# Optimization experiments

Hardware: AMD Instinct MI355X
Metric: run time of the kernel (lower is better)

The kernel has to match this reference:

```python
import jax, jax.numpy as jnp
import numpy as np

EPS = 0.01                      # cfg.eps
INV_4PI = 1.0 / (4.0 * np.pi)   # 3D free-space Green's constant


def setup_inputs() -> dict:
    key = jax.random.key(0)
    k1, k2, k3 = jax.random.split(key, 3)
    B, M, d = 32768, 2048, 3
    return {
        "x_query": jax.random.normal(k1, (B, d), dtype=jnp.float32),
        "x_land": jax.random.normal(k2, (M, d), dtype=jnp.float32),
        "g_land": jax.random.normal(k3, (M,), dtype=jnp.float32),
    }


def reference(x_query, x_land, g_land):
    # Regularized 3D Poisson Green's function:
    #   G(x,y)      =  1/(4*pi) * (||x-y||^2 + eps^2)^(-1/2)
    #   grad_x G    = -1/(4*pi) * (x-y) * (||x-y||^2 + eps^2)^(-3/2)
    M = x_land.shape[0]
    r2 = (jnp.sum(x_query * x_query, axis=1)[:, None]
          - 2.0 * (x_query @ x_land.T)
          + jnp.sum(x_land * x_land, axis=1)[None, :])
    t = jnp.maximum(r2, 0.0) + EPS * EPS          # (B, M), regularized
    G = INV_4PI * jax.lax.rsqrt(t)                # (B, M)
    v_hat = (G * g_land[None, :]).sum(axis=1) / M # (B,)
    # fused gradient reduction: avoid materializing (B, M, d) dG.
    # sum_m g_m * dG = -1/(4pi) * [ x_q * sum_m c_m  -  c @ x_land ],
    # where c_m = g_m * t^(-3/2)
    c = g_land[None, :] * t ** (-1.5)             # (B, M)
    gradv_hat = -INV_4PI * (x_query * c.sum(axis=1, keepdims=True) - c @ x_land) / M
    return v_hat, gradv_hat
```

## Files before the change

### kernel.cpp

```cpp
#include <hip/hip_runtime.h>
#include <math.h>


#define EPS2    1e-4f
#define INV_4PI 0.07957747154594767f

constexpr int M_LAND = 2048;
constexpr int NW     = 16;
constexpr int SLICE  = M_LAND / NW;
constexpr int QPB    = 128;

typedef float f32x2 __attribute__((ext_vector_type(2)));

__global__ __launch_bounds__(1024, 4)
void poisson_pk_kernel(const float* __restrict__ xq,
                       const float* __restrict__ xl,
                       const float* __restrict__ gl,
                       float* __restrict__ out, int B)
{
    __shared__ float4 pack[M_LAND];
    __shared__ float4 gpack[M_LAND];
    __shared__ float  part[NW][QPB][5];

    const int tid = threadIdx.x;

    for (int j = tid; j < M_LAND; j += 1024) {
        float l0 = xl[3*j], l1 = xl[3*j+1], l2 = xl[3*j+2], g = gl[j];
        float n2 = l0*l0 + l1*l1 + l2*l2 + EPS2;
        pack[j]  = make_float4(-2.0f*l0, -2.0f*l1, -2.0f*l2, n2);
        gpack[j] = make_float4(-2.0f*g*l0, -2.0f*g*l1, -2.0f*g*l2, g);
    }

    const int lane  = tid & 63;
    const int w     = tid >> 6;
    const int qbase = blockIdx.x * QPB;
    const int qa    = qbase + lane;
    const int qb    = qbase + 64 + lane;

    const float a0 = xq[3*qa], a1 = xq[3*qa+1], a2 = xq[3*qa+2];
    const float b0 = xq[3*qb], b1 = xq[3*qb+1], b2 = xq[3*qb+2];

    f32x2 Q0 = {a0, b0}, Q1 = {a1, b1}, Q2 = {a2, b2};
    f32x2 QE = {a0*a0 + a1*a1 + a2*a2, b0*b0 + b1*b1 + b2*b2};
    f32x2 AV = {0.f,0.f}, AC = {0.f,0.f}, AX = {0.f,0.f}, AY = {0.f,0.f}, AZ = {0.f,0.f};

    __syncthreads();

    const int base = w * SLICE;
#pragma unroll 8
    for (int i = 0; i < SLICE; ++i) {
        const float4 p  = pack[base + i];
        const float4 gp = gpack[base + i];
        f32x2 P01 = {p.x,  p.y};
        f32x2 P2W = {p.z,  p.w};
        f32x2 G01 = {gp.x, gp.y};
        f32x2 G2G = {gp.z, gp.w};

        f32x2 T;
        asm("v_pk_add_f32 %0, %1, %2 op_sel:[0,1] op_sel_hi:[1,1]\n\t"
            "v_pk_fma_f32 %0, %2, %3, %0 op_sel:[0,0,0] op_sel_hi:[0,1,1]\n\t"
            "v_pk_fma_f32 %0, %4, %5, %0 op_sel:[1,0,0] op_sel_hi:[1,1,1]\n\t"
            "v_pk_fma_f32 %0, %4, %6, %0 op_sel:[0,0,0] op_sel_hi:[0,1,1]"
            : "=&v"(T)
            : "v"(QE), "v"(P2W), "v"(Q2), "v"(P01), "v"(Q1), "v"(Q0));

        float ta = fmaxf(T.x, EPS2);
        float tb = fmaxf(T.y, EPS2);
        f32x2 S = { __builtin_amdgcn_rsqf(ta), __builtin_amdgcn_rsqf(tb) };

        f32x2 S2, S3;
        asm("v_pk_mul_f32 %0, %7, %7 op_sel:[0,0] op_sel_hi:[1,1]\n\t"
            "v_pk_mul_f32 %1, %0, %7 op_sel:[0,0] op_sel_hi:[1,1]\n\t"
            "v_pk_fma_f32 %2, %8, %7, %2 op_sel:[1,0,0] op_sel_hi:[1,1,1]\n\t"
            "v_pk_fma_f32 %3, %8, %1, %3 op_sel:[1,0,0] op_sel_hi:[1,1,1]\n\t"
            "v_pk_fma_f32 %4, %1, %9, %4 op_sel:[0,0,0] op_sel_hi:[1,0,1]\n\t"
            "v_pk_fma_f32 %5, %1, %9, %5 op_sel:[0,1,0] op_sel_hi:[1,1,1]\n\t"
            "v_pk_fma_f32 %6, %1, %8, %6 op_sel:[0,0,0] op_sel_hi:[1,0,1]"
            : "=&v"(S2), "=&v"(S3),
              "+v"(AV), "+v"(AC), "+v"(AX), "+v"(AY), "+v"(AZ)
            : "v"(S), "v"(G2G), "v"(G01));
    }

    part[w][lane][0] = AV.x;  part[w][lane][1] = AC.x;
    part[w][lane][2] = AX.x;  part[w][lane][3] = AY.x;  part[w][lane][4] = AZ.x;
    part[w][lane+64][0] = AV.y;  part[w][lane+64][1] = AC.y;
    part[w][lane+64][2] = AX.y;  part[w][lane+64][3] = AY.y;  part[w][lane+64][4] = AZ.y;

    __syncthreads();

    if (tid < 512) {
        const int q   = tid >> 2;
        const int cmp = tid & 3;
        const int qg  = qbase + q;
        if (cmp == 0) {
            float s = 0.f;
            #pragma unroll
            for (int ww = 0; ww < NW; ++ww) s += part[ww][q][0];
            out[qg] = s * (INV_4PI / (float)M_LAND);
        } else {
            float sc = 0.f, sy = 0.f;
            #pragma unroll
            for (int ww = 0; ww < NW; ++ww) {
                sc += part[ww][q][1];
                sy += part[ww][q][1 + cmp];
            }
            const float qc = xq[3*qg + (cmp-1)];
            out[B + 3*qg + (cmp-1)] =
                (-INV_4PI / (float)M_LAND) * fmaf(qc, sc, 0.5f * sy);
        }
    }
}

extern "C" void kernel_launch(void* const* d_in, const int* in_sizes, int n_in,
                              void* d_out, int out_size, void* d_ws, size_t ws_size,
                              hipStream_t stream)
{
    const float* xq = (const float*)d_in[0];
    const float* xl = (const float*)d_in[1];
    const float* gl = (const float*)d_in[2];
    float* out = (float*)d_out;

    const int B    = in_sizes[0] / 3;
    const int grid = B / QPB;

    poisson_pk_kernel<<<grid, 1024, 0, stream>>>(xq, xl, gl, out, B);
}
```

Baseline: 26.91 us.

## Store raw landmarks in one shared array and recompute norms per iteration

Drops the second shared-memory array of pre-scaled g*l values and the precomputed landmark norm. The -2 factor moves onto the query side, and each landmark's squared norm is recomputed inside the inner loop. Accumulation switches from inline-asm packed FMA to scalar code. This halves LDS reads and LDS footprint per iteration but adds about three FMAs per landmark plus extra scalar multiplies, and it gives up the explicit packed-math instructions.

```diff
diff --git a/kernel.cpp b/kernel.cpp
--- a/kernel.cpp
+++ b/kernel.cpp
@@ -13,23 +13,17 @@
 typedef float f32x2 __attribute__((ext_vector_type(2)));
 
 __global__ __launch_bounds__(1024, 4)
-void poisson_pk_kernel(const float* __restrict__ xq,
+void poisson_r7_kernel(const float* __restrict__ xq,
                        const float* __restrict__ xl,
                        const float* __restrict__ gl,
                        float* __restrict__ out, int B)
 {
     __shared__ float4 pack[M_LAND];
-    __shared__ float4 gpack[M_LAND];
     __shared__ float  part[NW][QPB][5];
 
     const int tid = threadIdx.x;
-
-    for (int j = tid; j < M_LAND; j += 1024) {
-        float l0 = xl[3*j], l1 = xl[3*j+1], l2 = xl[3*j+2], g = gl[j];
-        float n2 = l0*l0 + l1*l1 + l2*l2 + EPS2;
-        pack[j]  = make_float4(-2.0f*l0, -2.0f*l1, -2.0f*l2, n2);
-        gpack[j] = make_float4(-2.0f*g*l0, -2.0f*g*l1, -2.0f*g*l2, g);
-    }
+    for (int j = tid; j < M_LAND; j += 1024)
+        pack[j] = make_float4(xl[3*j], xl[3*j+1], xl[3*j+2], gl[j]);
 
     const int lane  = tid & 63;
     const int w     = tid >> 6;
@@ -40,51 +34,53 @@
     const float a0 = xq[3*qa], a1 = xq[3*qa+1], a2 = xq[3*qa+2];
     const float b0 = xq[3*qb], b1 = xq[3*qb+1], b2 = xq[3*qb+2];
 
-    f32x2 Q0 = {a0, b0}, Q1 = {a1, b1}, Q2 = {a2, b2};
-    f32x2 QE = {a0*a0 + a1*a1 + a2*a2, b0*b0 + b1*b1 + b2*b2};
-    f32x2 AV = {0.f,0.f}, AC = {0.f,0.f}, AX = {0.f,0.f}, AY = {0.f,0.f}, AZ = {0.f,0.f};
+    f32x2 Qn0 = {-2.0f*a0, -2.0f*b0};
+    f32x2 Qn1 = {-2.0f*a1, -2.0f*b1};
+    f32x2 Qn2 = {-2.0f*a2, -2.0f*b2};
+    f32x2 QE  = {a0*a0 + a1*a1 + a2*a2, b0*b0 + b1*b1 + b2*b2};
+
+    float av_a=0.f, ac_a=0.f, ax_a=0.f, ay_a=0.f, az_a=0.f;
+    float av_b=0.f, ac_b=0.f, ax_b=0.f, ay_b=0.f, az_b=0.f;
 
     __syncthreads();
 
     const int base = w * SLICE;
 #pragma unroll 8
     for (int i = 0; i < SLICE; ++i) {
-        const float4 p  = pack[base + i];
-        const float4 gp = gpack[base + i];
-        f32x2 P01 = {p.x,  p.y};
-        f32x2 P2W = {p.z,  p.w};
-        f32x2 G01 = {gp.x, gp.y};
-        f32x2 G2G = {gp.z, gp.w};
+        const float4 p = pack[base + i];
+        f32x2 P01 = {p.x, p.y};
+        f32x2 P2G = {p.z, p.w};
+
+        float n2 = fmaf(p.x, p.x, fmaf(p.y, p.y, fmaf(p.z, p.z, EPS2)));
 
         f32x2 T;
-        asm("v_pk_add_f32 %0, %1, %2 op_sel:[0,1] op_sel_hi:[1,1]\n\t"
-            "v_pk_fma_f32 %0, %2, %3, %0 op_sel:[0,0,0] op_sel_hi:[0,1,1]\n\t"
+        asm("v_pk_fma_f32 %0, %1, %2, %3 op_sel:[0,0,0] op_sel_hi:[0,1,1]\n\t"
             "v_pk_fma_f32 %0, %4, %5, %0 op_sel:[1,0,0] op_sel_hi:[1,1,1]\n\t"
             "v_pk_fma_f32 %0, %4, %6, %0 op_sel:[0,0,0] op_sel_hi:[0,1,1]"
             : "=&v"(T)
-            : "v"(QE), "v"(P2W), "v"(Q2), "v"(P01), "v"(Q1), "v"(Q0));
+            : "v"(P2G), "v"(Qn2), "v"(QE), "v"(P01), "v"(Qn1), "v"(Qn0));
 
-        float ta = fmaxf(T.x, EPS2);
-        float tb = fmaxf(T.y, EPS2);
-        f32x2 S = { __builtin_amdgcn_rsqf(ta), __builtin_amdgcn_rsqf(tb) };
+        float ta = fmaxf(T.x + n2, EPS2);
+        float tb = fmaxf(T.y + n2, EPS2);
+        float sa = __builtin_amdgcn_rsqf(ta);
+        float sb = __builtin_amdgcn_rsqf(tb);
 
-        f32x2 S2, S3;
-        asm("v_pk_mul_f32 %0, %7, %7 op_sel:[0,0] op_sel_hi:[1,1]\n\t"
-            "v_pk_mul_f32 %1, %0, %7 op_sel:[0,0] op_sel_hi:[1,1]\n\t"
-            "v_pk_fma_f32 %2, %8, %7, %2 op_sel:[1,0,0] op_sel_hi:[1,1,1]\n\t"
-            "v_pk_fma_f32 %3, %8, %1, %3 op_sel:[1,0,0] op_sel_hi:[1,1,1]\n\t"
-            "v_pk_fma_f32 %4, %1, %9, %4 op_sel:[0,0,0] op_sel_hi:[1,0,1]\n\t"
-            "v_pk_fma_f32 %5, %1, %9, %5 op_sel:[0,1,0] op_sel_hi:[1,1,1]\n\t"
-            "v_pk_fma_f32 %6, %1, %8, %6 op_sel:[0,0,0] op_sel_hi:[1,0,1]"
-            : "=&v"(S2), "=&v"(S3),
-              "+v"(AV), "+v"(AC), "+v"(AX), "+v"(AY), "+v"(AZ)
-            : "v"(S), "v"(G2G), "v"(G01));
+        float s3a = sa * sa * sa;
+        float s3b = sb * sb * sb;
+        float ca  = p.w * s3a;
+        float cb  = p.w * s3b;
+
+        av_a = fmaf(p.w, sa, av_a);   av_b = fmaf(p.w, sb, av_b);
+        ac_a += ca;                   ac_b += cb;
+        ax_a = fmaf(ca, p.x, ax_a);   ax_b = fmaf(cb, p.x, ax_b);
+        ay_a = fmaf(ca, p.y, ay_a);   ay_b = fmaf(cb, p.y, ay_b);
+        az_a = fmaf(ca, p.z, az_a);   az_b = fmaf(cb, p.z, az_b);
     }
 
-    part[w][lane][0] = AV.x;  part[w][lane][1] = AC.x;
-    part[w][lane][2] = AX.x;  part[w][lane][3] = AY.x;  part[w][lane][4] = AZ.x;
-    part[w][lane+64][0] = AV.y;  part[w][lane+64][1] = AC.y;
-    part[w][lane+64][2] = AX.y;  part[w][lane+64][3] = AY.y;  part[w][lane+64][4] = AZ.y;
+    part[w][lane][0] = av_a;  part[w][lane][1] = ac_a;
+    part[w][lane][2] = ax_a;  part[w][lane][3] = ay_a;  part[w][lane][4] = az_a;
+    part[w][lane+64][0] = av_b;  part[w][lane+64][1] = ac_b;
+    part[w][lane+64][2] = ax_b;  part[w][lane+64][3] = ay_b;  part[w][lane+64][4] = az_b;
 
     __syncthreads();
 
@@ -106,7 +102,7 @@
             }
             const float qc = xq[3*qg + (cmp-1)];
             out[B + 3*qg + (cmp-1)] =
-                (-INV_4PI / (float)M_LAND) * fmaf(qc, sc, 0.5f * sy);
+                (-INV_4PI / (float)M_LAND) * fmaf(qc, sc, -sy);
         }
     }
 }
@@ -123,5 +119,5 @@
     const int B    = in_sizes[0] / 3;
     const int grid = B / QPB;
 
-    poisson_pk_kernel<<<grid, 1024, 0, stream>>>(xq, xl, gl, out, B);
+    poisson_r7_kernel<<<grid, 1024, 0, stream>>>(xq, xl, gl, out, B);
 }
```

After: 31.22 us. 16.0% more time.

## Split landmark dimension across blocks with workspace partials and a combine kernel

Applied to the files above, without the earlier changes.

The work is now split into two kernels. The first gives each block 256 queries and one quarter of the landmarks, with every thread handling four queries, and writes reduced partial sums to the workspace. A second small kernel adds the four landmark-slice partials and forms the value and gradient outputs. The aim is to raise per-thread ILP, shrink the per-block shared-memory staging, and fill the GPU with 512 smaller blocks. The cost is an extra launch and a global-memory round trip, and the new path only runs when B equals 32768 and the workspace is large enough; otherwise the original kernel is used.

```diff
diff --git a/kernel.cpp b/kernel.cpp
--- a/kernel.cpp
+++ b/kernel.cpp
@@ -6,101 +6,199 @@
 #define INV_4PI 0.07957747154594767f
 
 constexpr int M_LAND = 2048;
-constexpr int NW     = 16;
-constexpr int SLICE  = M_LAND / NW;
-constexpr int QPB    = 128;
 
 typedef float f32x2 __attribute__((ext_vector_type(2)));
 
-__global__ __launch_bounds__(1024, 4)
-void poisson_pk_kernel(const float* __restrict__ xq,
-                       const float* __restrict__ xl,
-                       const float* __restrict__ gl,
-                       float* __restrict__ out, int B)
-{
-    __shared__ float4 pack[M_LAND];
-    __shared__ float4 gpack[M_LAND];
-    __shared__ float  part[NW][QPB][5];
-
-    const int tid = threadIdx.x;
-
-    for (int j = tid; j < M_LAND; j += 1024) {
-        float l0 = xl[3*j], l1 = xl[3*j+1], l2 = xl[3*j+2], g = gl[j];
+#define PAIR_COMPUTE(Q0_, Q1_, Q2_, QE_, AV_, AC_, AX_, AY_, AZ_) do { \
+    f32x2 T; \
+    asm("v_pk_add_f32 %0, %1, %2 op_sel:[0,1] op_sel_hi:[1,1]\n\t" \
+        "v_pk_fma_f32 %0, %2, %3, %0 op_sel:[0,0,0] op_sel_hi:[0,1,1]\n\t" \
+        "v_pk_fma_f32 %0, %4, %5, %0 op_sel:[1,0,0] op_sel_hi:[1,1,1]\n\t" \
+        "v_pk_fma_f32 %0, %4, %6, %0 op_sel:[0,0,0] op_sel_hi:[0,1,1]" \
+        : "=&v"(T) \
+        : "v"(QE_), "v"(P2W), "v"(Q2_), "v"(P01), "v"(Q1_), "v"(Q0_)); \
+    float ta = fmaxf(T.x, EPS2); \
+    float tb = fmaxf(T.y, EPS2); \
+    f32x2 S = { __builtin_amdgcn_rsqf(ta), __builtin_amdgcn_rsqf(tb) }; \
+    f32x2 S2, S3; \
+    asm("v_pk_mul_f32 %0, %7, %7 op_sel:[0,0] op_sel_hi:[1,1]\n\t" \
+        "v_pk_mul_f32 %1, %0, %7 op_sel:[0,0] op_sel_hi:[1,1]\n\t" \
+        "v_pk_fma_f32 %2, %8, %7, %2 op_sel:[1,0,0] op_sel_hi:[1,1,1]\n\t" \
+        "v_pk_fma_f32 %3, %8, %1, %3 op_sel:[1,0,0] op_sel_hi:[1,1,1]\n\t" \
+        "v_pk_fma_f32 %4, %1, %9, %4 op_sel:[0,0,0] op_sel_hi:[1,0,1]\n\t" \
+        "v_pk_fma_f32 %5, %1, %9, %5 op_sel:[0,1,0] op_sel_hi:[1,1,1]\n\t" \
+        "v_pk_fma_f32 %6, %1, %8, %6 op_sel:[0,0,0] op_sel_hi:[1,0,1]" \
+        : "=&v"(S2), "=&v"(S3), \
+          "+v"(AV_), "+v"(AC_), "+v"(AX_), "+v"(AY_), "+v"(AZ_) \
+        : "v"(S), "v"(G2G), "v"(G01)); \
+} while (0)
+
+__global__ __launch_bounds__(512, 4)
+void poisson_part_kernel(const float* __restrict__ xq,
+                         const float* __restrict__ xl,
+                         const float* __restrict__ gl,
+                         float* __restrict__ ws)
+{
+    __shared__ float4 pack[512];
+    __shared__ float4 gpack[512];
+    __shared__ float  part[8][256][5];
+
+    const int tid  = threadIdx.x;
+    const int qblk = blockIdx.x >> 2;
+    const int ms   = blockIdx.x & 3;
+
+    {
+        int jg = ms * 512 + tid;
+        float l0 = xl[3*jg], l1 = xl[3*jg+1], l2 = xl[3*jg+2], g = gl[jg];
         float n2 = l0*l0 + l1*l1 + l2*l2 + EPS2;
-        pack[j]  = make_float4(-2.0f*l0, -2.0f*l1, -2.0f*l2, n2);
-        gpack[j] = make_float4(-2.0f*g*l0, -2.0f*g*l1, -2.0f*g*l2, g);
+        pack[tid]  = make_float4(-2.0f*l0, -2.0f*l1, -2.0f*l2, n2);
+        gpack[tid] = make_float4(-2.0f*g*l0, -2.0f*g*l1, -2.0f*g*l2, g);
     }
 
     const int lane  = tid & 63;
     const int w     = tid >> 6;
-    const int qbase = blockIdx.x * QPB;
-    const int qa    = qbase + lane;
-    const int qb    = qbase + 64 + lane;
+    const int qbase = qblk * 256;
+
+    const int qa = qbase + lane,       qbq = qbase + 64  + lane;
+    const int qc = qbase + 128 + lane, qd  = qbase + 192 + lane;
 
     const float a0 = xq[3*qa], a1 = xq[3*qa+1], a2 = xq[3*qa+2];
-    const float b0 = xq[3*qb], b1 = xq[3*qb+1], b2 = xq[3*qb+2];
-
-    f32x2 Q0 = {a0, b0}, Q1 = {a1, b1}, Q2 = {a2, b2};
-    f32x2 QE = {a0*a0 + a1*a1 + a2*a2, b0*b0 + b1*b1 + b2*b2};
-    f32x2 AV = {0.f,0.f}, AC = {0.f,0.f}, AX = {0.f,0.f}, AY = {0.f,0.f}, AZ = {0.f,0.f};
-
-    __syncthreads();
-
-    const int base = w * SLICE;
-#pragma unroll 8
-    for (int i = 0; i < SLICE; ++i) {
+    const float b0 = xq[3*qbq], b1 = xq[3*qbq+1], b2 = xq[3*qbq+2];
+    const float c0 = xq[3*qc], c1 = xq[3*qc+1], c2 = xq[3*qc+2];
+    const float d0 = xq[3*qd], d1 = xq[3*qd+1], d2 = xq[3*qd+2];
+
+    f32x2 Q0a = {a0, b0}, Q1a = {a1, b1}, Q2a = {a2, b2};
+    f32x2 QEa = {a0*a0 + a1*a1 + a2*a2, b0*b0 + b1*b1 + b2*b2};
+    f32x2 Q0b = {c0, d0}, Q1b = {c1, d1}, Q2b = {c2, d2};
+    f32x2 QEb = {c0*c0 + c1*c1 + c2*c2, d0*d0 + d1*d1 + d2*d2};
+
+    f32x2 AVa = {0,0}, ACa = {0,0}, AXa = {0,0}, AYa = {0,0}, AZa = {0,0};
+    f32x2 AVb = {0,0}, ACb = {0,0}, AXb = {0,0}, AYb = {0,0}, AZb = {0,0};
+
+    __syncthreads();
+
+    const int base = w * 64;
+#pragma unroll 4
+    for (int i = 0; i < 64; ++i) {
         const float4 p  = pack[base + i];
         const float4 gp = gpack[base + i];
         f32x2 P01 = {p.x,  p.y};
         f32x2 P2W = {p.z,  p.w};
         f32x2 G01 = {gp.x, gp.y};
         f32x2 G2G = {gp.z, gp.w};
-
-        f32x2 T;
-        asm("v_pk_add_f32 %0, %1, %2 op_sel:[0,1] op_sel_hi:[1,1]\n\t"
-            "v_pk_fma_f32 %0, %2, %3, %0 op_sel:[0,0,0] op_sel_hi:[0,1,1]\n\t"
-            "v_pk_fma_f32 %0, %4, %5, %0 op_sel:[1,0,0] op_sel_hi:[1,1,1]\n\t"
-            "v_pk_fma_f32 %0, %4, %6, %0 op_sel:[0,0,0] op_sel_hi:[0,1,1]"
-            : "=&v"(T)
-            : "v"(QE), "v"(P2W), "v"(Q2), "v"(P01), "v"(Q1), "v"(Q0));
-
-        float ta = fmaxf(T.x, EPS2);
-        float tb = fmaxf(T.y, EPS2);
-        f32x2 S = { __builtin_amdgcn_rsqf(ta), __builtin_amdgcn_rsqf(tb) };
-
-        f32x2 S2, S3;
-        asm("v_pk_mul_f32 %0, %7, %7 op_sel:[0,0] op_sel_hi:[1,1]\n\t"
-            "v_pk_mul_f32 %1, %0, %7 op_sel:[0,0] op_sel_hi:[1,1]\n\t"
-            "v_pk_fma_f32 %2, %8, %7, %2 op_sel:[1,0,0] op_sel_hi:[1,1,1]\n\t"
-            "v_pk_fma_f32 %3, %8, %1, %3 op_sel:[1,0,0] op_sel_hi:[1,1,1]\n\t"
-            "v_pk_fma_f32 %4, %1, %9, %4 op_sel:[0,0,0] op_sel_hi:[1,0,1]\n\t"
-            "v_pk_fma_f32 %5, %1, %9, %5 op_sel:[0,1,0] op_sel_hi:[1,1,1]\n\t"
-            "v_pk_fma_f32 %6, %1, %8, %6 op_sel:[0,0,0] op_sel_hi:[1,0,1]"
-            : "=&v"(S2), "=&v"(S3),
-              "+v"(AV), "+v"(AC), "+v"(AX), "+v"(AY), "+v"(AZ)
-            : "v"(S), "v"(G2G), "v"(G01));
-    }
-
+        PAIR_COMPUTE(Q0a, Q1a, Q2a, QEa, AVa, ACa, AXa, AYa, AZa);
+        PAIR_COMPUTE(Q0b, Q1b, Q2b, QEb, AVb, ACb, AXb, AYb, AZb);
+    }
+
+    part[w][lane][0] = AVa.x;  part[w][lane][1] = ACa.x;
+    part[w][lane][2] = AXa.x;  part[w][lane][3] = AYa.x;  part[w][lane][4] = AZa.x;
+    part[w][lane+64][0] = AVa.y;  part[w][lane+64][1] = ACa.y;
+    part[w][lane+64][2] = AXa.y;  part[w][lane+64][3] = AYa.y;  part[w][lane+64][4] = AZa.y;
+    part[w][lane+128][0] = AVb.x;  part[w][lane+128][1] = ACb.x;
+    part[w][lane+128][2] = AXb.x;  part[w][lane+128][3] = AYb.x;  part[w][lane+128][4] = AZb.x;
+    part[w][lane+192][0] = AVb.y;  part[w][lane+192][1] = ACb.y;
+    part[w][lane+192][2] = AXb.y;  part[w][lane+192][3] = AYb.y;  part[w][lane+192][4] = AZb.y;
+
+    __syncthreads();
+
+    for (int s = tid; s < 1280; s += 512) {
+        const int comp = s >> 8;
+        const int qloc = s & 255;
+        float acc = 0.f;
+        #pragma unroll
+        for (int ww = 0; ww < 8; ++ww) acc += part[ww][qloc][comp];
+        ws[(size_t)blockIdx.x * 1280 + s] = acc;
+    }
+}
+
+__global__ __launch_bounds__(512)
+void poisson_combine_kernel(const float* __restrict__ ws,
+                            const float* __restrict__ xq,
+                            float* __restrict__ out, int B)
+{
+    const int gid  = blockIdx.x * 512 + threadIdx.x;
+    const int q    = gid >> 2;
+    const int cmp  = gid & 3;
+    const int qblk = q >> 8;
+    const int qloc = q & 255;
+    const float* wbase = ws + (size_t)qblk * 4 * 1280;
+
+    if (cmp == 0) {
+        float s = 0.f;
+        #pragma unroll
+        for (int m = 0; m < 4; ++m) s += wbase[m*1280 + qloc];
+        out[q] = s * (INV_4PI / (float)M_LAND);
+    } else {
+        float sc = 0.f, sy = 0.f;
+        #pragma unroll
+        for (int m = 0; m < 4; ++m) {
+            sc += wbase[m*1280 + 256 + qloc];
+            sy += wbase[m*1280 + (1+cmp)*256 + qloc];
+        }
+        const float qc = xq[3*q + (cmp-1)];
+        out[B + 3*q + (cmp-1)] =
+            (-INV_4PI / (float)M_LAND) * fmaf(qc, sc, 0.5f * sy);
+    }
+}
+
+constexpr int NW_F  = 16;
+constexpr int SL_F  = M_LAND / NW_F;
+constexpr int QPB_F = 128;
+
+__global__ __launch_bounds__(1024, 4)
+void poisson_pk_kernel(const float* __restrict__ xq,
+                       const float* __restrict__ xl,
+                       const float* __restrict__ gl,
+                       float* __restrict__ out, int B)
+{
+    __shared__ float4 pack[M_LAND];
+    __shared__ float4 gpack[M_LAND];
+    __shared__ float  part[NW_F][QPB_F][5];
+
+    const int tid = threadIdx.x;
+    for (int j = tid; j < M_LAND; j += 1024) {
+        float l0 = xl[3*j], l1 = xl[3*j+1], l2 = xl[3*j+2], g = gl[j];
+        float n2 = l0*l0 + l1*l1 + l2*l2 + EPS2;
+        pack[j]  = make_float4(-2.0f*l0, -2.0f*l1, -2.0f*l2, n2);
+        gpack[j] = make_float4(-2.0f*g*l0, -2.0f*g*l1, -2.0f*g*l2, g);
+    }
+    const int lane = tid & 63, w = tid >> 6;
+    const int qbase = blockIdx.x * QPB_F;
+    const int qa = qbase + lane, qb = qbase + 64 + lane;
+    const float a0 = xq[3*qa], a1 = xq[3*qa+1], a2 = xq[3*qa+2];
+    const float b0 = xq[3*qb], b1 = xq[3*qb+1], b2 = xq[3*qb+2];
+    f32x2 Q0 = {a0, b0}, Q1 = {a1, b1}, Q2 = {a2, b2};
+    f32x2 QE = {a0*a0 + a1*a1 + a2*a2, b0*b0 + b1*b1 + b2*b2};
+    f32x2 AV = {0,0}, AC = {0,0}, AX = {0,0}, AY = {0,0}, AZ = {0,0};
+    __syncthreads();
+
+    const int base = w * SL_F;
+#pragma unroll 8
+    for (int i = 0; i < SL_F; ++i) {
+        const float4 p  = pack[base + i];
+        const float4 gp = gpack[base + i];
+        f32x2 P01 = {p.x,  p.y};
+        f32x2 P2W = {p.z,  p.w};
+        f32x2 G01 = {gp.x, gp.y};
+        f32x2 G2G = {gp.z, gp.w};
+        PAIR_COMPUTE(Q0, Q1, Q2, QE, AV, AC, AX, AY, AZ);
+    }
     part[w][lane][0] = AV.x;  part[w][lane][1] = AC.x;
     part[w][lane][2] = AX.x;  part[w][lane][3] = AY.x;  part[w][lane][4] = AZ.x;
     part[w][lane+64][0] = AV.y;  part[w][lane+64][1] = AC.y;
     part[w][lane+64][2] = AX.y;  part[w][lane+64][3] = AY.y;  part[w][lane+64][4] = AZ.y;
-
-    __syncthreads();
-
+    __syncthreads();
     if (tid < 512) {
-        const int q   = tid >> 2;
-        const int cmp = tid & 3;
-        const int qg  = qbase + q;
+        const int q = tid >> 2, cmp = tid & 3, qg = qbase + q;
         if (cmp == 0) {
             float s = 0.f;
             #pragma unroll
-            for (int ww = 0; ww < NW; ++ww) s += part[ww][q][0];
+            for (int ww = 0; ww < NW_F; ++ww) s += part[ww][q][0];
             out[qg] = s * (INV_4PI / (float)M_LAND);
         } else {
             float sc = 0.f, sy = 0.f;
             #pragma unroll
-            for (int ww = 0; ww < NW; ++ww) {
+            for (int ww = 0; ww < NW_F; ++ww) {
                 sc += part[ww][q][1];
                 sy += part[ww][q][1 + cmp];
             }
@@ -120,8 +218,14 @@
     const float* gl = (const float*)d_in[2];
     float* out = (float*)d_out;
 
-    const int B    = in_sizes[0] / 3;
-    const int grid = B / QPB;
-
-    poisson_pk_kernel<<<grid, 1024, 0, stream>>>(xq, xl, gl, out, B);
-}
+    const int B = in_sizes[0] / 3;
+
+    const size_t need = (size_t)512 * 1280 * sizeof(float);
+    if (ws_size >= need && B == 32768) {
+        float* ws = (float*)d_ws;
+        poisson_part_kernel<<<512, 512, 0, stream>>>(xq, xl, gl, ws);
+        poisson_combine_kernel<<<256, 512, 0, stream>>>(ws, xq, out, B);
+    } else {
+        poisson_pk_kernel<<<B / QPB_F, 1024, 0, stream>>>(xq, xl, gl, out, B);
+    }
+}
```

New measurement: 28.09 us. +4.4%, slower.
